# Kernel tuning notes

Hardware: AMD Instinct MI355X
Metric: run time of the kernel (lower is better)

The kernel has to match this reference:

```python
import jax, jax.numpy as jnp
import numpy as np

DIMS = [1024, 2048, 2048, 51]
B, P = 16, 1024


def setup_inputs() -> dict:
    key = jax.random.key(0)
    ks = jax.random.split(key, 1 + 2 * (len(DIMS) - 1))
    inp = {
        "num_pairs": P,
        "classifier_input": jax.random.normal(ks[0], (B, P, DIMS[0]), dtype=jnp.float32),
        "num_batches": B,
    }
    # Linear params, PyTorch-style: W[out, in], b[out]
    for li in range(len(DIMS) - 1):
        fan_in = DIMS[li]
        bound = 1.0 / np.sqrt(fan_in)
        inp[f"W{li}"] = jax.random.uniform(ks[1 + 2 * li], (DIMS[li + 1], fan_in), minval=-bound, maxval=bound, dtype=jnp.float32)
        inp[f"b{li}"] = jax.random.uniform(ks[2 + 2 * li], (DIMS[li + 1],), minval=-bound, maxval=bound, dtype=jnp.float32)
    return inp


def reference(num_pairs, classifier_input, num_batches, W0, b0, W1, b1, W2, b2):
    # Batched MLP over all (num_batches * num_pairs) vectors at once.
    # Original loops per (b, i); math is identical. dropout p=0.0 -> identity.
    x = classifier_input  # [B, P, d_in]
    x = jax.nn.relu(jnp.einsum("bpd,hd->bph", x, W0) + b0)
    x = jax.nn.relu(jnp.einsum("bpd,hd->bph", x, W1) + b1)
    out = jnp.einsum("bpd,od->bpo", x, W2) + b2  # [B, P, n_classes]
    return out
```

## Files before the change

### kernel.cpp

```cpp
#include <hip/hip_runtime.h>
#include <hip/hip_bf16.h>
#include <stdint.h>

typedef __attribute__((ext_vector_type(8))) short short8;
typedef __attribute__((ext_vector_type(8))) uint16_t ushort8;
typedef __attribute__((ext_vector_type(4))) float floatx4;

#define TK 64


__device__ __forceinline__ uint16_t f2bf_bits(float f) {
    uint32_t u = __builtin_bit_cast(uint32_t, f);
    u += 0x7FFFu + ((u >> 16) & 1u);
    return (uint16_t)(u >> 16);
}

__device__ __forceinline__ void async_copy16(const void* g, void* l) {
    auto gp = (const __attribute__((address_space(1))) uint32_t*)(uintptr_t)g;
    auto lp = (__attribute__((address_space(3))) uint32_t*)(uint32_t)(uintptr_t)l;
    __builtin_amdgcn_global_load_lds(gp, lp, 16, 0, 0);
}


__global__ void cvt8(const float* __restrict__ src, uint16_t* __restrict__ dst, int n) {
    int i = (blockIdx.x * 256 + threadIdx.x) * 8;
    if (i >= n) return;
    floatx4 a = *(const floatx4*)(src + i);
    floatx4 b = *(const floatx4*)(src + i + 4);
    ushort8 o;
#pragma unroll
    for (int k = 0; k < 4; k++) {
        o[k]     = f2bf_bits(a[k]);
        o[k + 4] = f2bf_bits(b[k]);
    }
    *(ushort8*)(dst + i) = o;
}

__global__ void cvt_pad_w2(const float* __restrict__ src, uint16_t* __restrict__ dst) {
    int i = (blockIdx.x * 256 + threadIdx.x) * 8;
    int row = i >> 11;
    ushort8 o;
    if (row < 51) {
        floatx4 a = *(const floatx4*)(src + i);
        floatx4 b = *(const floatx4*)(src + i + 4);
#pragma unroll
        for (int k = 0; k < 4; k++) {
            o[k]     = f2bf_bits(a[k]);
            o[k + 4] = f2bf_bits(b[k]);
        }
    } else {
#pragma unroll
        for (int k = 0; k < 8; k++) o[k] = 0;
    }
    *(ushort8*)(dst + i) = o;
}


template <int MI, int NJ, bool RELU, bool OUTF32>
__global__ __launch_bounds__(256, 2)
void gemm_bt(const uint16_t* __restrict__ A,
             const uint16_t* __restrict__ W,
             const float* __restrict__ bias,
             void* __restrict__ out,
             int M, int N, int K, int ldc, int nstore)
{
    constexpr int TMv = MI * 32;
    constexpr int TNv = NJ * 32;
    constexpr int ACH = TMv / 32;
    constexpr int BCH = TNv / 32;

    __shared__ alignas(16) uint16_t sA[TMv * TK];
    __shared__ alignas(16) uint16_t sB[TNv * TK];

    const int tid  = threadIdx.x;
    const int wave = tid >> 6;
    const int lane = tid & 63;

    const int f   = blockIdx.x;
    const int xcd = f & 7;
    const int loc = f >> 3;
    const int per = (int)gridDim.x >> 3;
    const int nt  = N / TNv;
    const int n_t = loc % nt;
    const int m_t = xcd * (per / nt) + loc / nt;
    const int n0 = n_t * TNv;
    const int m0 = m_t * TMv;

    floatx4 acc[MI][NJ];
    const floatx4 zero = {0.f, 0.f, 0.f, 0.f};
#pragma unroll
    for (int i = 0; i < MI; i++)
#pragma unroll
        for (int j = 0; j < NJ; j++) acc[i][j] = zero;

    const int wr = (wave >> 1) * MI * 16;
    const int wc = (wave & 1) * NJ * 16;

    const int sr   = lane >> 3;
    const int scol = ((lane & 7) ^ sr) * 8;

    const uint16_t* ap[ACH];
    const uint16_t* bp[BCH];
#pragma unroll
    for (int t = 0; t < ACH; t++)
        ap[t] = A + (size_t)(m0 + (wave + 4 * t) * 8 + sr) * K + scol;
#pragma unroll
    for (int t = 0; t < BCH; t++)
        bp[t] = W + (size_t)(n0 + (wave + 4 * t) * 8 + sr) * K + scol;

    const int fm = lane & 15;
    const int fr = fm & 7;
    const int kgb = lane >> 4;

    const int niter = K / TK;
    for (int it = 0; it < niter; it++) {
#pragma unroll
        for (int t = 0; t < ACH; t++) {
            async_copy16(ap[t], sA + (wave + 4 * t) * 512);
            ap[t] += TK;
        }
#pragma unroll
        for (int t = 0; t < BCH; t++) {
            async_copy16(bp[t], sB + (wave + 4 * t) * 512);
            bp[t] += TK;
        }
        __syncthreads();

#pragma unroll
        for (int kk = 0; kk < 2; kk++) {
            const int slot = ((kgb + 4 * kk) ^ fr) * 8;
            short8 af[MI], bfr[NJ];
#pragma unroll
            for (int i = 0; i < MI; i++)
                af[i] = *(const short8*)(sA + (wr + i * 16 + fm) * TK + slot);
#pragma unroll
            for (int j = 0; j < NJ; j++)
                bfr[j] = *(const short8*)(sB + (wc + j * 16 + fm) * TK + slot);
#pragma unroll
            for (int i = 0; i < MI; i++)
#pragma unroll
                for (int j = 0; j < NJ; j++)
                    acc[i][j] = __builtin_amdgcn_mfma_f32_16x16x32_bf16(af[i], bfr[j], acc[i][j], 0, 0, 0);
        }
        __syncthreads();
    }

    const int cr = (lane >> 4) * 4;
    const int cc = lane & 15;
#pragma unroll
    for (int i = 0; i < MI; i++) {
        const int gmb = m0 + wr + i * 16 + cr;
#pragma unroll
        for (int j = 0; j < NJ; j++) {
            const int gn = n0 + wc + j * 16 + cc;
            if (gn < nstore) {
                const float bv = bias[gn];
#pragma unroll
                for (int r = 0; r < 4; r++) {
                    float v = acc[i][j][r] + bv;
                    if (RELU) v = fmaxf(v, 0.f);
                    const size_t idx = (size_t)(gmb + r) * ldc + gn;
                    if (OUTF32) ((float*)out)[idx] = v;
                    else        ((uint16_t*)out)[idx] = f2bf_bits(v);
                }
            }
        }
    }
}


#define SCHED0 __builtin_amdgcn_sched_barrier(0)

#define LOAD_A(SA, QM) do { \
    const uint16_t* _p = (SA) + (QM) * 8192 + aoff; \
    _Pragma("unroll") \
    for (int kk = 0; kk < 2; kk++) { \
      const int sl = ((kgb + 4 * kk) ^ fr) * 8; \
      _Pragma("unroll") \
      for (int mi = 0; mi < 4; mi++) \
        af[mi][kk] = *(const short8*)(_p + mi * 1024 + sl); \
    } } while (0)

#define LOAD_B(SB, QN, BF) do { \
    const uint16_t* _p = (SB) + (QN) * 8192 + boff; \
    _Pragma("unroll") \
    for (int kk = 0; kk < 2; kk++) { \
      const int sl = ((kgb + 4 * kk) ^ fr) * 8; \
      _Pragma("unroll") \
      for (int nj = 0; nj < 2; nj++) \
        BF[nj][kk] = *(const short8*)(_p + nj * 1024 + sl); \
    } } while (0)

#define PH_MFMA(QM, QN, BF) \
    SCHED0; \
    __builtin_amdgcn_s_barrier(); \
    asm volatile("s_waitcnt lgkmcnt(0)" ::: "memory"); \
    SCHED0; \
    __builtin_amdgcn_s_setprio(1); \
    _Pragma("unroll") \
    for (int kk = 0; kk < 2; kk++) \
      _Pragma("unroll") \
      for (int mi = 0; mi < 4; mi++) \
        _Pragma("unroll") \
        for (int nj = 0; nj < 2; nj++) \
          acc[QM][QN][mi][nj] = __builtin_amdgcn_mfma_f32_16x16x32_bf16( \
              af[mi][kk], BF[nj][kk], acc[QM][QN][mi][nj], 0, 0, 0); \
    __builtin_amdgcn_s_setprio(0); \
    SCHED0; \
    __builtin_amdgcn_s_barrier(); \
    SCHED0;

#define ITER_BODY(T, LAST) \
     \
    LOAD_A(sA0, 0); \
    LOAD_B(sB0, 0, b0); \
    stA(1, (T) + 1, sA1); \
    asm volatile("s_waitcnt lgkmcnt(8)"); \
    PH_MFMA(0, 0, b0); \
     \
    LOAD_B(sB0, 1, b1); \
    if (!(LAST)) stA(0, (T) + 2, sA0); \
    PH_MFMA(0, 1, b1); \
     \
    LOAD_A(sA0, 1); \
    if (!(LAST)) stB(0, (T) + 2, sB0); \
    PH_MFMA(1, 1, b1); \
     \
    if (!(LAST)) { \
      stB(1, (T) + 2, sB0); \
      asm volatile("s_waitcnt vmcnt(6)" ::: "memory"); \
    } else { \
      asm volatile("s_waitcnt vmcnt(0)" ::: "memory"); \
    } \
    PH_MFMA(1, 0, b0); \
     \
    LOAD_A(sA1, 0); \
    LOAD_B(sB1, 0, b0); \
    if (!(LAST)) stA(1, (T) + 2, sA0); \
    asm volatile("s_waitcnt lgkmcnt(8)"); \
    PH_MFMA(0, 0, b0); \
     \
    LOAD_B(sB1, 1, b1); \
    if (!(LAST)) stA(0, (T) + 3, sA1); \
    PH_MFMA(0, 1, b1); \
     \
    LOAD_A(sA1, 1); \
    if (!(LAST)) stB(0, (T) + 3, sB1); \
    PH_MFMA(1, 1, b1); \
     \
    if (!(LAST)) { \
      stB(1, (T) + 3, sB1); \
      asm volatile("s_waitcnt vmcnt(6)" ::: "memory"); \
    } \
    PH_MFMA(1, 0, b0);

template <bool RELU, bool OUTF32>
__global__ __launch_bounds__(512, 2)
void gemm256(const uint16_t* __restrict__ A,
             const uint16_t* __restrict__ W,
             const float* __restrict__ bias,
             void* __restrict__ out,
             int K, int N, int ldc, int nstore)
{
    extern __shared__ uint16_t smem[];
    uint16_t* sA0 = smem;
    uint16_t* sA1 = smem + 16384;
    uint16_t* sB0 = smem + 32768;
    uint16_t* sB1 = smem + 49152;

    const int tid  = threadIdx.x;
    const int wave = tid >> 6;
    const int lane = tid & 63;
    const int wm2  = wave >> 2;
    const int wn2  = wave & 3;

    const int f   = blockIdx.x;
    const int xcd = f & 7;
    const int loc = f >> 3;
    const int per = (int)gridDim.x >> 3;
    const int ntn = N / 256;
    const int n_t = loc % ntn;
    const int m_t = xcd * (per / ntn) + loc / ntn;
    const int m0 = m_t * 256;
    const int n0 = n_t * 256;

    floatx4 acc[2][2][4][2];
    const floatx4 zero = {0.f, 0.f, 0.f, 0.f};
#pragma unroll
    for (int qm = 0; qm < 2; qm++)
#pragma unroll
    for (int qn = 0; qn < 2; qn++)
#pragma unroll
    for (int mi = 0; mi < 4; mi++)
#pragma unroll
    for (int nj = 0; nj < 2; nj++) acc[qm][qn][mi][nj] = zero;

    const int srow = lane >> 3;
    const int scol = ((lane & 7) ^ srow) * 8;
    const uint16_t* pA = A + (size_t)(m0 + wave * 8 + srow) * K + scol;
    const uint16_t* pB = W + (size_t)(n0 + wave * 8 + srow) * K + scol;

    auto stA = [&](int h, int kt, uint16_t* buf) {
        const uint16_t* p = pA + (size_t)h * 128 * K + (size_t)kt * 64;
        async_copy16(p,                  buf + h * 8192 + wave * 512);
        async_copy16(p + (size_t)64 * K, buf + h * 8192 + 4096 + wave * 512);
    };
    auto stB = [&](int h, int kt, uint16_t* buf) {
        const uint16_t* p = pB + (size_t)h * 128 * K + (size_t)kt * 64;
        async_copy16(p,                  buf + h * 8192 + wave * 512);
        async_copy16(p + (size_t)64 * K, buf + h * 8192 + 4096 + wave * 512);
    };

    const int fm  = lane & 15;
    const int fr  = fm & 7;
    const int kgb = lane >> 4;
    const int aoff = (wm2 * 64 + fm) * 64;
    const int boff = (wn2 * 32 + fm) * 64;

    short8 af[4][2];
    short8 b0[2][2];
    short8 b1[2][2];

    stA(0, 0, sA0);
    stB(0, 0, sB0);
    stA(1, 0, sA0);
    stB(1, 0, sB0);
    stA(0, 1, sA1);
    stB(0, 1, sB1);
    stB(1, 1, sB1);
    asm volatile("s_waitcnt vmcnt(6)" ::: "memory");
    __builtin_amdgcn_s_barrier();
    SCHED0;

    const int niter2 = K / 128;
    for (int it = 0; it < niter2 - 1; ++it) {
        const int T = 2 * it;
        ITER_BODY(T, false);
    }
    {
        const int T = 2 * (niter2 - 1);
        ITER_BODY(T, true);
    }

    const int cr = (lane >> 4) * 4;
    const int cc = lane & 15;
#pragma unroll
    for (int qm = 0; qm < 2; qm++)
#pragma unroll
    for (int mi = 0; mi < 4; mi++) {
        const int gm = m0 + qm * 128 + wm2 * 64 + mi * 16 + cr;
#pragma unroll
        for (int qn = 0; qn < 2; qn++)
#pragma unroll
        for (int nj = 0; nj < 2; nj++) {
            const int gn = n0 + qn * 128 + wn2 * 32 + nj * 16 + cc;
            if (gn < nstore) {
                const float bv = bias[gn];
#pragma unroll
                for (int r = 0; r < 4; r++) {
                    float v = acc[qm][qn][mi][nj][r] + bv;
                    if (RELU) v = fmaxf(v, 0.f);
                    const size_t idx = (size_t)(gm + r) * ldc + gn;
                    if (OUTF32) ((float*)out)[idx] = v;
                    else        ((uint16_t*)out)[idx] = f2bf_bits(v);
                }
            }
        }
    }
}


extern "C" void kernel_launch(void* const* d_in, const int* in_sizes, int n_in,
                              void* d_out, int out_size, void* d_ws, size_t ws_size,
                              hipStream_t stream) {
    (void)in_sizes; (void)n_in; (void)out_size; (void)ws_size;
    const float* X  = (const float*)d_in[1];
    const float* W0 = (const float*)d_in[3];
    const float* b0 = (const float*)d_in[4];
    const float* W1 = (const float*)d_in[5];
    const float* b1 = (const float*)d_in[6];
    const float* W2 = (const float*)d_in[7];
    const float* b2 = (const float*)d_in[8];

    const int M = 16384;

    static bool attr_done = false;
    if (!attr_done) {
        (void)hipFuncSetAttribute((const void*)gemm256<true, false>,
                                  hipFuncAttributeMaxDynamicSharedMemorySize, 131072);
        attr_done = true;
    }

    char* w = (char*)d_ws;
    uint16_t* X0  = (uint16_t*)w; w += (size_t)M * 1024 * 2;
    uint16_t* X1  = (uint16_t*)w; w += (size_t)M * 2048 * 2;
    uint16_t* X2  = (uint16_t*)w; w += (size_t)M * 2048 * 2;
    uint16_t* W0b = (uint16_t*)w; w += (size_t)2048 * 1024 * 2;
    uint16_t* W1b = (uint16_t*)w; w += (size_t)2048 * 2048 * 2;
    uint16_t* W2b = (uint16_t*)w; w += (size_t)64 * 2048 * 2;

    cvt8<<<M * 1024 / 8 / 256, 256, 0, stream>>>(X, X0, M * 1024);
    cvt8<<<2048 * 1024 / 8 / 256, 256, 0, stream>>>(W0, W0b, 2048 * 1024);
    cvt8<<<2048 * 2048 / 8 / 256, 256, 0, stream>>>(W1, W1b, 2048 * 2048);
    cvt_pad_w2<<<64 * 2048 / 8 / 256, 256, 0, stream>>>(W2, W2b);

    gemm256<true, false><<<dim3((M / 256) * (2048 / 256)), 512, 131072, stream>>>(
        X0, W0b, b0, X1, 1024, 2048, 2048, 2048);
    gemm256<true, false><<<dim3((M / 256) * (2048 / 256)), 512, 131072, stream>>>(
        X1, W1b, b1, X2, 2048, 2048, 2048, 2048);
    gemm_bt<1, 2, false, true><<<dim3(M / 32), 256, 0, stream>>>(
        X2, W2b, b2, d_out, M, 64, 2048, 51, 51);
}
```

Before: 349.1 us.

## Restructure GEMM main loop to one barrier per K-tile with register-prefetched A fragments

```diff
diff --git a/kernel.cpp b/kernel.cpp
--- a/kernel.cpp
+++ b/kernel.cpp
@@ -171,17 +171,17 @@
 
 #define SCHED0 __builtin_amdgcn_sched_barrier(0)
 
-#define LOAD_A(SA, QM) do { \
+#define LOAD_AF(SA, QM, DST) do { \
     const uint16_t* _p = (SA) + (QM) * 8192 + aoff; \
     _Pragma("unroll") \
     for (int kk = 0; kk < 2; kk++) { \
       const int sl = ((kgb + 4 * kk) ^ fr) * 8; \
       _Pragma("unroll") \
       for (int mi = 0; mi < 4; mi++) \
-        af[mi][kk] = *(const short8*)(_p + mi * 1024 + sl); \
+        DST[mi][kk] = *(const short8*)(_p + mi * 1024 + sl); \
     } } while (0)
 
-#define LOAD_B(SB, QN, BF) do { \
+#define LOAD_BF(SB, QN, BF) do { \
     const uint16_t* _p = (SB) + (QN) * 8192 + boff; \
     _Pragma("unroll") \
     for (int kk = 0; kk < 2; kk++) { \
@@ -191,11 +191,7 @@
         BF[nj][kk] = *(const short8*)(_p + nj * 1024 + sl); \
     } } while (0)
 
-#define PH_MFMA(QM, QN, BF) \
-    SCHED0; \
-    __builtin_amdgcn_s_barrier(); \
-    asm volatile("s_waitcnt lgkmcnt(0)" ::: "memory"); \
-    SCHED0; \
+#define MFMA_CL(QM, QN, AF, BF) \
     __builtin_amdgcn_s_setprio(1); \
     _Pragma("unroll") \
     for (int kk = 0; kk < 2; kk++) \
@@ -204,55 +200,28 @@
         _Pragma("unroll") \
         for (int nj = 0; nj < 2; nj++) \
           acc[QM][QN][mi][nj] = __builtin_amdgcn_mfma_f32_16x16x32_bf16( \
-              af[mi][kk], BF[nj][kk], acc[QM][QN][mi][nj], 0, 0, 0); \
+              AF[mi][kk], BF[nj][kk], acc[QM][QN][mi][nj], 0, 0, 0); \
     __builtin_amdgcn_s_setprio(0); \
+    SCHED0;
+
+#define TILE_BODY(SAC, SBC, SAN, TT, STG, NEXT) \
+     \
+    LOAD_BF(SBC, 0, b0); \
+    LOAD_BF(SBC, 1, b1); \
+    LOAD_AF(SAC, 1, aQ); \
+    SCHED0; \
+    MFMA_CL(0, 0, aP, b0); \
+    MFMA_CL(0, 1, aP, b1); \
+    asm volatile("s_waitcnt vmcnt(0) lgkmcnt(0)" ::: "memory"); \
     SCHED0; \
     __builtin_amdgcn_s_barrier(); \
-    SCHED0;
-
-#define ITER_BODY(T, LAST) \
+    SCHED0; \
      \
-    LOAD_A(sA0, 0); \
-    LOAD_B(sB0, 0, b0); \
-    stA(1, (T) + 1, sA1); \
-    asm volatile("s_waitcnt lgkmcnt(8)"); \
-    PH_MFMA(0, 0, b0); \
-     \
-    LOAD_B(sB0, 1, b1); \
-    if (!(LAST)) stA(0, (T) + 2, sA0); \
-    PH_MFMA(0, 1, b1); \
-     \
-    LOAD_A(sA0, 1); \
-    if (!(LAST)) stB(0, (T) + 2, sB0); \
-    PH_MFMA(1, 1, b1); \
-     \
-    if (!(LAST)) { \
-      stB(1, (T) + 2, sB0); \
-      asm volatile("s_waitcnt vmcnt(6)" ::: "memory"); \
-    } else { \
-      asm volatile("s_waitcnt vmcnt(0)" ::: "memory"); \
-    } \
-    PH_MFMA(1, 0, b0); \
-     \
-    LOAD_A(sA1, 0); \
-    LOAD_B(sB1, 0, b0); \
-    if (!(LAST)) stA(1, (T) + 2, sA0); \
-    asm volatile("s_waitcnt lgkmcnt(8)"); \
-    PH_MFMA(0, 0, b0); \
-     \
-    LOAD_B(sB1, 1, b1); \
-    if (!(LAST)) stA(0, (T) + 3, sA1); \
-    PH_MFMA(0, 1, b1); \
-     \
-    LOAD_A(sA1, 1); \
-    if (!(LAST)) stB(0, (T) + 3, sB1); \
-    PH_MFMA(1, 1, b1); \
-     \
-    if (!(LAST)) { \
-      stB(1, (T) + 3, sB1); \
-      asm volatile("s_waitcnt vmcnt(6)" ::: "memory"); \
-    } \
-    PH_MFMA(1, 0, b0);
+    if (STG) { stB((TT) + 2, SBC); stA((TT) + 2, SAC); } \
+    if (NEXT) LOAD_AF(SAN, 0, aP); \
+    SCHED0; \
+    MFMA_CL(1, 0, aQ, b0); \
+    MFMA_CL(1, 1, aQ, b1);
 
 template <bool RELU, bool OUTF32>
 __global__ __launch_bounds__(512, 2)
@@ -300,15 +269,19 @@
     const uint16_t* pA = A + (size_t)(m0 + wave * 8 + srow) * K + scol;
     const uint16_t* pB = W + (size_t)(n0 + wave * 8 + srow) * K + scol;
 
-    auto stA = [&](int h, int kt, uint16_t* buf) {
-        const uint16_t* p = pA + (size_t)h * 128 * K + (size_t)kt * 64;
-        async_copy16(p,                  buf + h * 8192 + wave * 512);
-        async_copy16(p + (size_t)64 * K, buf + h * 8192 + 4096 + wave * 512);
+    auto stA = [&](int kt, uint16_t* buf) {
+        const uint16_t* p = pA + (size_t)kt * 64;
+        async_copy16(p,                    buf + wave * 512);
+        async_copy16(p + (size_t)64  * K,  buf + 4096  + wave * 512);
+        async_copy16(p + (size_t)128 * K,  buf + 8192  + wave * 512);
+        async_copy16(p + (size_t)192 * K,  buf + 12288 + wave * 512);
     };
-    auto stB = [&](int h, int kt, uint16_t* buf) {
-        const uint16_t* p = pB + (size_t)h * 128 * K + (size_t)kt * 64;
-        async_copy16(p,                  buf + h * 8192 + wave * 512);
-        async_copy16(p + (size_t)64 * K, buf + h * 8192 + 4096 + wave * 512);
+    auto stB = [&](int kt, uint16_t* buf) {
+        const uint16_t* p = pB + (size_t)kt * 64;
+        async_copy16(p,                    buf + wave * 512);
+        async_copy16(p + (size_t)64  * K,  buf + 4096  + wave * 512);
+        async_copy16(p + (size_t)128 * K,  buf + 8192  + wave * 512);
+        async_copy16(p + (size_t)192 * K,  buf + 12288 + wave * 512);
     };
 
     const int fm  = lane & 15;
@@ -317,30 +290,28 @@
     const int aoff = (wm2 * 64 + fm) * 64;
     const int boff = (wn2 * 32 + fm) * 64;
 
-    short8 af[4][2];
+    short8 aP[4][2];
+    short8 aQ[4][2];
     short8 b0[2][2];
     short8 b1[2][2];
 
-    stA(0, 0, sA0);
-    stB(0, 0, sB0);
-    stA(1, 0, sA0);
-    stB(1, 0, sB0);
-    stA(0, 1, sA1);
-    stB(0, 1, sB1);
-    stB(1, 1, sB1);
-    asm volatile("s_waitcnt vmcnt(6)" ::: "memory");
+    stB(0, sB0);
+    stA(0, sA0);
+    stB(1, sB1);
+    stA(1, sA1);
+    asm volatile("s_waitcnt vmcnt(8)" ::: "memory");
     __builtin_amdgcn_s_barrier();
     SCHED0;
-
-    const int niter2 = K / 128;
-    for (int it = 0; it < niter2 - 1; ++it) {
+    LOAD_AF(sA0, 0, aP);
+
+    const int niter = K / 64;
+    for (int it = 0; it < (niter - 2) / 2; ++it) {
         const int T = 2 * it;
-        ITER_BODY(T, false);
-    }
-    {
-        const int T = 2 * (niter2 - 1);
-        ITER_BODY(T, true);
-    }
+        TILE_BODY(sA0, sB0, sA1, T,     true, true);
+        TILE_BODY(sA1, sB1, sA0, T + 1, true, true);
+    }
+    TILE_BODY(sA0, sB0, sA1, niter - 2, false, true);
+    TILE_BODY(sA1, sB1, sA0, niter - 1, false, false);
 
     const int cr = (lane >> 4) * 4;
     const int cc = lane & 15;
```

After: 640.7 us. 1.84x slower.
